# Kernel tuning notes

Measured on AMD Instinct MI355X. Metric: run time of the kernel, lower is better.

Reference implementation:

```python
import jax, jax.numpy as jnp
import numpy as np

B, S, D, H, DH = 2, 2048, 1024, 16, 64
SCALE = float(np.sqrt(DH))
IGNORE = -100000.0


def setup_inputs() -> dict:
    key = jax.random.key(0)
    ks = jax.random.split(key, 9)
    s = 0.02
    return {
        "x": jax.random.normal(ks[0], (B, S, D), dtype=jnp.float32),
        "W_Q": jax.random.normal(ks[1], (H, DH, D), dtype=jnp.float32) * s,
        "W_K": jax.random.normal(ks[2], (H, DH, D), dtype=jnp.float32) * s,
        "W_V": jax.random.normal(ks[3], (H, DH, D), dtype=jnp.float32) * s,
        "W_O": jax.random.normal(ks[4], (H, D, DH), dtype=jnp.float32) * s,
        "b_Q": jax.random.normal(ks[5], (H, DH), dtype=jnp.float32) * s,
        "b_K": jax.random.normal(ks[6], (H, DH), dtype=jnp.float32) * s,
        "b_V": jax.random.normal(ks[7], (H, DH), dtype=jnp.float32) * s,
        "b_O": jax.random.normal(ks[8], (D,), dtype=jnp.float32) * s,
        "mask": jnp.tril(jnp.ones((S, S), dtype=bool)),  # causal, global attn_type
    }


def reference(x, W_Q, W_K, W_V, W_O, b_Q, b_K, b_V, b_O, mask):
    # q,k,v: [batch, pos, head, d_head]
    q = jnp.einsum('ihm,bpm->bpih', W_Q, x) + b_Q
    k = jnp.einsum('ihm,bpm->bpih', W_K, x) + b_K
    v = jnp.einsum('ihm,bpm->bpih', W_V, x) + b_V
    # scores: [batch, head, q_pos, k_pos]
    attn_scores = jnp.einsum('bpih,bqih->bipq', q, k) / SCALE
    attn_scores = jnp.where(mask, attn_scores, IGNORE)
    attn = jax.nn.softmax(attn_scores, axis=-1)
    # z: [batch, q_pos, head, d_head]
    z = jnp.einsum('bpih,biqp->bqih', v, attn)
    out = jnp.einsum('idh,bqih->bqd', W_O, z) + b_O
    return out
```

## Files before the change

kernel.cpp:

```cpp
#include <hip/hip_runtime.h>
#include <stdint.h>

typedef __attribute__((ext_vector_type(8))) short bf16x8;
typedef __attribute__((ext_vector_type(4))) float f32x4;
typedef __attribute__((ext_vector_type(16))) float f32x16;
typedef __attribute__((ext_vector_type(4))) unsigned short us4;

#define LOG2E 1.44269504088896340736f

__device__ __forceinline__ unsigned short f2bf(float f) {
    union { float f; unsigned u; } v; v.f = f;
    unsigned r = v.u + 0x7FFFu + ((v.u >> 16) & 1u);
    return (unsigned short)(r >> 16);
}
__device__ __forceinline__ float bf2f(unsigned short u) {
    return __uint_as_float(((unsigned)u) << 16);
}

__device__ __forceinline__ unsigned cvtpk(float lo, float hi) {
    unsigned r;
    asm("v_cvt_pk_bf16_f32 %0, %1, %2" : "=v"(r) : "v"(lo), "v"(hi));
    return r;
}
__device__ __forceinline__ void plswap(unsigned &a, unsigned &b) {
    asm volatile("v_permlane32_swap_b32 %0, %1" : "+v"(a), "+v"(b));
}

__device__ __forceinline__ void gld16(const void* g, void* l) {
    __builtin_amdgcn_global_load_lds((const __attribute__((address_space(1))) void*)g,
                                     (__attribute__((address_space(3))) void*)l, 16, 0, 0);
}

__global__ void k_cvt(const float* __restrict__ in, unsigned short* __restrict__ out, int n4) {
    int i = blockIdx.x * blockDim.x + threadIdx.x;
    if (i >= n4) return;
    float4 v = ((const float4*)in)[i];
    us4 o; o.x = f2bf(v.x); o.y = f2bf(v.y); o.z = f2bf(v.z); o.w = f2bf(v.w);
    *(us4*)(out + (size_t)i * 4) = o;
}

__global__ void k_cvt_wo(const float* __restrict__ WO, unsigned short* __restrict__ out) {
    int t = blockIdx.x * blockDim.x + threadIdx.x;
    int d = t >> 10, nn = t & 1023, i = nn >> 6, h = nn & 63;
    out[t] = f2bf(WO[(((size_t)i << 10) + d) * 64 + h]);
}

__global__ __launch_bounds__(256) void k_gemm_qkv(
    const unsigned short* __restrict__ Xb,
    const unsigned short* __restrict__ Wq, const unsigned short* __restrict__ Wk,
    const unsigned short* __restrict__ Wv,
    const float* __restrict__ bQ, const float* __restrict__ bK, const float* __restrict__ bV,
    unsigned short* __restrict__ Qb, unsigned short* __restrict__ Kb, unsigned short* __restrict__ VTb)
{
    __shared__ unsigned short As[128][64];
    __shared__ unsigned short Bs[128][64];
    const int which = blockIdx.z;
    const unsigned short* Wp = which == 0 ? Wq : (which == 1 ? Wk : Wv);
    const int bm = blockIdx.x, bn = blockIdx.y;
    const int t = threadIdx.x, lane = t & 63, wave = t >> 6;
    const int wm = wave >> 1, wn = wave & 1;
    const int l15 = lane & 15, l4 = lane >> 4;
    const int rsw = l15 & 7;
    f32x4 acc[4][4] = {};
    for (int k0 = 0; k0 < 1024; k0 += 64) {
        #pragma unroll
        for (int it = 0; it < 4; ++it) {
            int c = it * 256 + wave * 64 + lane;
            int row = c >> 3, sl = (c & 7) ^ (row & 7);
            gld16(Xb + ((bm << 7) + row) * 1024 + k0 + sl * 8, (char*)As + ((it * 256 + wave * 64) << 4));
            gld16(Wp + ((bn << 7) + row) * 1024 + k0 + sl * 8, (char*)Bs + ((it * 256 + wave * 64) << 4));
        }
        __syncthreads();
        const char* Ab = (const char*)As;
        const char* Bb = (const char*)Bs;
        #pragma unroll
        for (int kk = 0; kk < 2; ++kk) {
            bf16x8 af[4], bfg[4];
            #pragma unroll
            for (int m = 0; m < 4; ++m)
                af[m] = *(const bf16x8*)(Ab + (wm * 64 + m * 16 + l15) * 128 + (((kk * 4 + l4) ^ rsw) << 4));
            #pragma unroll
            for (int n = 0; n < 4; ++n)
                bfg[n] = *(const bf16x8*)(Bb + (wn * 64 + n * 16 + l15) * 128 + (((kk * 4 + l4) ^ rsw) << 4));
            #pragma unroll
            for (int m = 0; m < 4; ++m)
                #pragma unroll
                for (int n = 0; n < 4; ++n)
                    acc[m][n] = __builtin_amdgcn_mfma_f32_16x16x32_bf16(af[m], bfg[n], acc[m][n], 0, 0, 0);
        }
        __syncthreads();
    }
    #pragma unroll
    for (int m = 0; m < 4; ++m) {
        #pragma unroll
        for (int n = 0; n < 4; ++n) {
            int col = (bn << 7) + wn * 64 + n * 16 + l15;
            int i = col >> 6, h = col & 63;
            float bias = which == 0 ? bQ[col] : (which == 1 ? bK[col] : bV[col]);
            #pragma unroll
            for (int r = 0; r < 4; ++r) {
                int p = (bm << 7) + wm * 64 + m * 16 + (l4 << 2) + r;
                int b = p >> 11, s = p & 2047;
                float v = acc[m][n][r] + bias;
                if (which == 0)
                    Qb[(((((size_t)b << 4) + i) << 11) + s) * 64 + h] = f2bf(v * (0.125f * LOG2E));
                else if (which == 1)
                    Kb[(((((size_t)b << 4) + i) << 11) + s) * 64 + h] = f2bf(v);
                else
                    VTb[(((((size_t)b << 4) + i) << 6) + h) * 2048 + s] = f2bf(v);
            }
        }
    }
}

__global__ __launch_bounds__(128) void k_attn(
    const unsigned short* __restrict__ Qb, const unsigned short* __restrict__ Kb,
    const unsigned short* __restrict__ VTb,
    unsigned short* __restrict__ Zp, float* __restrict__ Lse)
{
    __shared__ __align__(16) char Lbuf[16384];
    const int id = (int)blockIdx.x;
    const int bi = id & 31;
    const int r = id >> 5;
    const int c = 31 - (r >> 1);
    const int part = r & 1;
    const int n = c + 1, n0 = (n + 1) >> 1;
    const int t0 = part ? n0 : 0, t1 = part ? n : n0;
    const int lane = threadIdx.x & 63, w = threadIdx.x >> 6;
    const int l31 = lane & 31, hi = lane >> 5;
    const unsigned short* Qh = Qb + (size_t)bi * 2048 * 64;
    const char* Khb = (const char*)(Kb + (size_t)bi * 2048 * 64);
    const char* Vhb = (const char*)(VTb + (size_t)bi * 64 * 2048);
    const int q0 = c * 64 + w * 32;
    const int q = q0 + l31;

    bf16x8 qf[4];
    #pragma unroll
    for (int kk = 0; kk < 4; ++kk)
        qf[kk] = *(const bf16x8*)&Qh[(size_t)q * 64 + kk * 16 + hi * 8];

    const int r8 = lane >> 3;
    const int swz = ((lane & 7) * 16) ^ (r8 << 4);
    const int koff = r8 * 128 + swz;
    const int voff = r8 * 4096 + swz;

    const int rsw = (l31 & 7) << 4;
    int kaddr[8];
    #pragma unroll
    for (int i = 0; i < 8; ++i)
        kaddr[i] = (l31 + 32 * (i >> 2)) * 128 + ((32 * (i & 3) + 16 * hi) ^ rsw);
    int vcol[4];
    #pragma unroll
    for (int f = 0; f < 4; ++f)
        vcol[f] = ((f * 32 + 16 * hi) ^ rsw);

    f32x16 za0 = {}, za1 = {};
    float m_run = -1e30f, l_run = 0.f;

    if (t0 < t1) {
        if (w == 0) {
            const char* src = Khb + (size_t)t0 * 8192 + koff;
            #pragma unroll
            for (int it = 0; it < 8; ++it) gld16(src + it * 1024, &Lbuf[0] + it * 1024);
        } else {
            const char* src = Vhb + (size_t)t0 * 128 + voff;
            #pragma unroll
            for (int it = 0; it < 8; ++it) gld16(src + it * 32768, &Lbuf[8192] + it * 1024);
        }
    }

    for (int t = t0; t < t1; ++t) {
        __syncthreads();
        const char* KL = &Lbuf[0];
        const char* VL = &Lbuf[8192];
        bf16x8 ka[8];
        #pragma unroll
        for (int i = 0; i < 8; ++i) ka[i] = *(const bf16x8*)(KL + kaddr[i]);
        bf16x8 vf0[4], vf1[4];
        #pragma unroll
        for (int f = 0; f < 4; ++f) {
            vf0[f] = *(const bf16x8*)(VL + l31 * 128 + vcol[f]);
            vf1[f] = *(const bf16x8*)(VL + (l31 + 32) * 128 + vcol[f]);
        }
        __syncthreads();
        if (t + 1 < t1) {
            if (w == 0) {
                const char* src = Khb + (size_t)(t + 1) * 8192 + koff;
                #pragma unroll
                for (int it = 0; it < 8; ++it) gld16(src + it * 1024, &Lbuf[0] + it * 1024);
            } else {
                const char* src = Vhb + (size_t)(t + 1) * 128 + voff;
                #pragma unroll
                for (int it = 0; it < 8; ++it) gld16(src + it * 32768, &Lbuf[8192] + it * 1024);
            }
        }

        const bool full = !(t == c && w == 0);
        f32x16 s0 = {}, s1;
        __builtin_amdgcn_s_setprio(1);
        #pragma unroll
        for (int kk = 0; kk < 4; ++kk)
            s0 = __builtin_amdgcn_mfma_f32_32x32x16_bf16(ka[kk], qf[kk], s0, 0, 0, 0);
        if (full) {
            f32x16 z = {};
            #pragma unroll
            for (int kk = 0; kk < 4; ++kk)
                z = __builtin_amdgcn_mfma_f32_32x32x16_bf16(ka[4 + kk], qf[kk], z, 0, 0, 0);
            s1 = z;
        }
        __builtin_amdgcn_s_setprio(0);

        if (!full) {
            #pragma unroll
            for (int j = 0; j < 16; ++j) s1[j] = -100000.0f;
        }
        if (t == c) {
            #pragma unroll
            for (int j = 0; j < 16; ++j) {
                int kv0 = (j & 3) + 8 * (j >> 2) + 4 * hi;
                if (c * 64 + kv0 > q) s0[j] = -100000.0f;
                if (c * 64 + kv0 + 32 > q) s1[j] = -100000.0f;
            }
        }
        float tmax = -1e30f;
        #pragma unroll
        for (int j = 0; j < 16; ++j) tmax = fmaxf(tmax, fmaxf(s0[j], s1[j]));
        tmax = fmaxf(tmax, __shfl_xor(tmax, 32, 64));
        if (!__all(tmax <= m_run + 8.0f)) {
            float newm = fmaxf(m_run, tmax);
            float alpha = exp2f(m_run - newm);
            m_run = newm;
            l_run *= alpha;
            za0 *= alpha; za1 *= alpha;
        }
        float rsum = 0.f;
        #pragma unroll
        for (int j = 0; j < 16; ++j) { s0[j] = exp2f(s0[j] - m_run); rsum += s0[j]; }
        if (full) {
            #pragma unroll
            for (int j = 0; j < 16; ++j) { s1[j] = exp2f(s1[j] - m_run); rsum += s1[j]; }
        }
        rsum += __shfl_xor(rsum, 32, 64);
        l_run += rsum;

        union { unsigned u[4]; bf16x8 v; } pk0, pk1, pk2, pk3;
        {
            unsigned a0 = cvtpk(s0[0], s0[1]),  a1 = cvtpk(s0[2], s0[3]);
            unsigned a2 = cvtpk(s0[4], s0[5]),  a3 = cvtpk(s0[6], s0[7]);
            plswap(a0, a2); plswap(a1, a3);
            pk0.u[0] = a0; pk0.u[1] = a1; pk0.u[2] = a2; pk0.u[3] = a3;
            unsigned b0 = cvtpk(s0[8], s0[9]),  b1 = cvtpk(s0[10], s0[11]);
            unsigned b2 = cvtpk(s0[12], s0[13]), b3 = cvtpk(s0[14], s0[15]);
            plswap(b0, b2); plswap(b1, b3);
            pk1.u[0] = b0; pk1.u[1] = b1; pk1.u[2] = b2; pk1.u[3] = b3;
        }
        if (full) {
            unsigned a0 = cvtpk(s1[0], s1[1]),  a1 = cvtpk(s1[2], s1[3]);
            unsigned a2 = cvtpk(s1[4], s1[5]),  a3 = cvtpk(s1[6], s1[7]);
            plswap(a0, a2); plswap(a1, a3);
            pk2.u[0] = a0; pk2.u[1] = a1; pk2.u[2] = a2; pk2.u[3] = a3;
            unsigned b0 = cvtpk(s1[8], s1[9]),  b1 = cvtpk(s1[10], s1[11]);
            unsigned b2 = cvtpk(s1[12], s1[13]), b3 = cvtpk(s1[14], s1[15]);
            plswap(b0, b2); plswap(b1, b3);
            pk3.u[0] = b0; pk3.u[1] = b1; pk3.u[2] = b2; pk3.u[3] = b3;
        }
        __builtin_amdgcn_s_setprio(1);
        za0 = __builtin_amdgcn_mfma_f32_32x32x16_bf16(vf0[0], pk0.v, za0, 0, 0, 0);
        za1 = __builtin_amdgcn_mfma_f32_32x32x16_bf16(vf1[0], pk0.v, za1, 0, 0, 0);
        za0 = __builtin_amdgcn_mfma_f32_32x32x16_bf16(vf0[1], pk1.v, za0, 0, 0, 0);
        za1 = __builtin_amdgcn_mfma_f32_32x32x16_bf16(vf1[1], pk1.v, za1, 0, 0, 0);
        if (full) {
            za0 = __builtin_amdgcn_mfma_f32_32x32x16_bf16(vf0[2], pk2.v, za0, 0, 0, 0);
            za1 = __builtin_amdgcn_mfma_f32_32x32x16_bf16(vf1[2], pk2.v, za1, 0, 0, 0);
            za0 = __builtin_amdgcn_mfma_f32_32x32x16_bf16(vf0[3], pk3.v, za0, 0, 0, 0);
            za1 = __builtin_amdgcn_mfma_f32_32x32x16_bf16(vf1[3], pk3.v, za1, 0, 0, 0);
        }
        __builtin_amdgcn_s_setprio(0);
    }

    const float rl = (l_run > 0.f) ? 1.0f / l_run : 0.f;
    const float lse = (l_run > 0.f) ? m_run + log2f(l_run) : -1e30f;
    const int pb = (part << 5) + bi;
    unsigned short* zp = Zp + ((size_t)pb * 2048 + q) * 64;
    #pragma unroll
    for (int nn = 0; nn < 2; ++nn) {
        #pragma unroll
        for (int gg = 0; gg < 4; ++gg) {
            int dh0 = nn * 32 + 8 * gg + 4 * hi;
            us4 o;
            float v0 = (nn ? za1[4 * gg + 0] : za0[4 * gg + 0]) * rl;
            float v1 = (nn ? za1[4 * gg + 1] : za0[4 * gg + 1]) * rl;
            float v2 = (nn ? za1[4 * gg + 2] : za0[4 * gg + 2]) * rl;
            float v3 = (nn ? za1[4 * gg + 3] : za0[4 * gg + 3]) * rl;
            o.x = f2bf(v0); o.y = f2bf(v1); o.z = f2bf(v2); o.w = f2bf(v3);
            *(us4*)(zp + dh0) = o;
        }
    }
    if (hi == 0) Lse[(size_t)pb * 2048 + q] = lse;
}

__global__ __launch_bounds__(256) void k_combine(
    const unsigned short* __restrict__ Zp, const float* __restrict__ Lse,
    unsigned short* __restrict__ Zb)
{
    const int tid = blockIdx.x * 256 + threadIdx.x;
    const int dc = tid & 7, q = (tid >> 3) & 2047, bi = tid >> 14;
    const float l0 = Lse[(size_t)bi * 2048 + q];
    const float l1 = Lse[(size_t)(32 + bi) * 2048 + q];
    const float M = fmaxf(l0, l1);
    float e0 = exp2f(l0 - M), e1 = exp2f(l1 - M);
    const float rs = 1.0f / (e0 + e1);
    e0 *= rs; e1 *= rs;
    const size_t base = ((size_t)bi * 2048 + q) * 64 + dc * 8;
    bf16x8 z0 = *(const bf16x8*)(Zp + base);
    bf16x8 z1 = *(const bf16x8*)(Zp + (size_t)32 * 2048 * 64 + base);
    const int b = bi >> 4, ih = bi & 15;
    unsigned short* op = Zb + (((size_t)b * 2048 + q) << 10) + ih * 64 + dc * 8;
    bf16x8 o;
    #pragma unroll
    for (int j = 0; j < 8; ++j) {
        float v = e0 * bf2f((unsigned short)z0[j]) + e1 * bf2f((unsigned short)z1[j]);
        o[j] = (short)f2bf(v);
    }
    *(bf16x8*)op = o;
}

__global__ __launch_bounds__(256) void k_gemm_out(
    const unsigned short* __restrict__ Zb, const unsigned short* __restrict__ Wo,
    const float* __restrict__ bO, float* __restrict__ out)
{
    __shared__ unsigned short As[128][64];
    __shared__ unsigned short Bs[128][64];
    const int bm = blockIdx.x, bn = blockIdx.y;
    const int t = threadIdx.x, lane = t & 63, wave = t >> 6;
    const int wm = wave >> 1, wn = wave & 1;
    const int l15 = lane & 15, l4 = lane >> 4;
    const int rsw = l15 & 7;
    f32x4 acc[4][4] = {};
    for (int k0 = 0; k0 < 1024; k0 += 64) {
        #pragma unroll
        for (int it = 0; it < 4; ++it) {
            int c = it * 256 + wave * 64 + lane;
            int row = c >> 3, sl = (c & 7) ^ (row & 7);
            gld16(Zb + ((bm << 7) + row) * 1024 + k0 + sl * 8, (char*)As + ((it * 256 + wave * 64) << 4));
            gld16(Wo + ((bn << 7) + row) * 1024 + k0 + sl * 8, (char*)Bs + ((it * 256 + wave * 64) << 4));
        }
        __syncthreads();
        const char* Ab = (const char*)As;
        const char* Bb = (const char*)Bs;
        #pragma unroll
        for (int kk = 0; kk < 2; ++kk) {
            bf16x8 af[4], bfg[4];
            #pragma unroll
            for (int m = 0; m < 4; ++m)
                af[m] = *(const bf16x8*)(Ab + (wm * 64 + m * 16 + l15) * 128 + (((kk * 4 + l4) ^ rsw) << 4));
            #pragma unroll
            for (int n = 0; n < 4; ++n)
                bfg[n] = *(const bf16x8*)(Bb + (wn * 64 + n * 16 + l15) * 128 + (((kk * 4 + l4) ^ rsw) << 4));
            #pragma unroll
            for (int m = 0; m < 4; ++m)
                #pragma unroll
                for (int n = 0; n < 4; ++n)
                    acc[m][n] = __builtin_amdgcn_mfma_f32_16x16x32_bf16(af[m], bfg[n], acc[m][n], 0, 0, 0);
        }
        __syncthreads();
    }
    #pragma unroll
    for (int m = 0; m < 4; ++m) {
        #pragma unroll
        for (int n = 0; n < 4; ++n) {
            int col = (bn << 7) + wn * 64 + n * 16 + l15;
            float bias = bO[col];
            #pragma unroll
            for (int r = 0; r < 4; ++r) {
                int p = (bm << 7) + wm * 64 + m * 16 + (l4 << 2) + r;
                out[(size_t)p * 1024 + col] = acc[m][n][r] + bias;
            }
        }
    }
}

extern "C" void kernel_launch(void* const* d_in, const int* in_sizes, int n_in,
                              void* d_out, int out_size, void* d_ws, size_t ws_size,
                              hipStream_t stream)
{
    const float* x  = (const float*)d_in[0];
    const float* WQ = (const float*)d_in[1];
    const float* WK = (const float*)d_in[2];
    const float* WV = (const float*)d_in[3];
    const float* WO = (const float*)d_in[4];
    const float* bQ = (const float*)d_in[5];
    const float* bK = (const float*)d_in[6];
    const float* bV = (const float*)d_in[7];
    const float* bO = (const float*)d_in[8];
    float* out = (float*)d_out;

    char* w = (char*)d_ws;
    unsigned short* xb  = (unsigned short*)w; w += (size_t)4096 * 1024 * 2;
    unsigned short* wqb = (unsigned short*)w; w += (size_t)1024 * 1024 * 2;
    unsigned short* wkb = (unsigned short*)w; w += (size_t)1024 * 1024 * 2;
    unsigned short* wvb = (unsigned short*)w; w += (size_t)1024 * 1024 * 2;
    unsigned short* wob = (unsigned short*)w; w += (size_t)1024 * 1024 * 2;
    unsigned short* Qb  = (unsigned short*)w; w += (size_t)4096 * 1024 * 2;
    unsigned short* Kb  = (unsigned short*)w; w += (size_t)4096 * 1024 * 2;
    unsigned short* VTb = (unsigned short*)w; w += (size_t)4096 * 1024 * 2;
    unsigned short* Zb  = (unsigned short*)w; w += (size_t)4096 * 1024 * 2;
    unsigned short* Zp  = (unsigned short*)w; w += (size_t)2 * 32 * 2048 * 64 * 2;
    float*          Lse = (float*)w;          w += (size_t)2 * 32 * 2048 * 4;

    k_cvt<<<4096, 256, 0, stream>>>(x, xb, 1048576);
    k_cvt<<<1024, 256, 0, stream>>>(WQ, wqb, 262144);
    k_cvt<<<1024, 256, 0, stream>>>(WK, wkb, 262144);
    k_cvt<<<1024, 256, 0, stream>>>(WV, wvb, 262144);
    k_cvt_wo<<<4096, 256, 0, stream>>>(WO, wob);

    k_gemm_qkv<<<dim3(32, 8, 3), 256, 0, stream>>>(xb, wqb, wkb, wvb, bQ, bK, bV, Qb, Kb, VTb);
    k_attn<<<2048, 128, 0, stream>>>(Qb, Kb, VTb, Zp, Lse);
    k_combine<<<2048, 256, 0, stream>>>(Zp, Lse, Zb);
    k_gemm_out<<<dim3(32, 8), 256, 0, stream>>>(Zb, wob, bO, out);
}
```

Measured before the change: 141.1 us.

## Double-buffer LDS tiles in QKV and output GEMMs, merge weight conversions

Both projection GEMMs now use two LDS buffers, so the global-to-LDS loads for the next K-slice are issued before the MFMA work on the current slice, overlapping memory latency with compute. One barrier per iteration is dropped. The three Q/K/V weight conversion launches are merged into a single 2D-grid launch to cut launch overhead. LDS use per block doubles to 64KB, which may reduce the number of blocks resident per CU.

```diff
diff --git a/kernel.cpp b/kernel.cpp
--- a/kernel.cpp
+++ b/kernel.cpp
@@ -34,6 +34,18 @@
 __global__ void k_cvt(const float* __restrict__ in, unsigned short* __restrict__ out, int n4) {
     int i = blockIdx.x * blockDim.x + threadIdx.x;
     if (i >= n4) return;
+    float4 v = ((const float4*)in)[i];
+    us4 o; o.x = f2bf(v.x); o.y = f2bf(v.y); o.z = f2bf(v.z); o.w = f2bf(v.w);
+    *(us4*)(out + (size_t)i * 4) = o;
+}
+
+__global__ void k_cvt3(const float* __restrict__ a, const float* __restrict__ b,
+                       const float* __restrict__ cc,
+                       unsigned short* __restrict__ oa, unsigned short* __restrict__ ob,
+                       unsigned short* __restrict__ oc) {
+    const float* in = blockIdx.y == 0 ? a : (blockIdx.y == 1 ? b : cc);
+    unsigned short* out = blockIdx.y == 0 ? oa : (blockIdx.y == 1 ? ob : oc);
+    int i = blockIdx.x * blockDim.x + threadIdx.x;
     float4 v = ((const float4*)in)[i];
     us4 o; o.x = f2bf(v.x); o.y = f2bf(v.y); o.z = f2bf(v.z); o.w = f2bf(v.w);
     *(us4*)(out + (size_t)i * 4) = o;
@@ -52,8 +64,8 @@
     const float* __restrict__ bQ, const float* __restrict__ bK, const float* __restrict__ bV,
     unsigned short* __restrict__ Qb, unsigned short* __restrict__ Kb, unsigned short* __restrict__ VTb)
 {
-    __shared__ unsigned short As[128][64];
-    __shared__ unsigned short Bs[128][64];
+    __shared__ unsigned short As[2][128][64];
+    __shared__ unsigned short Bs[2][128][64];
     const int which = blockIdx.z;
     const unsigned short* Wp = which == 0 ? Wq : (which == 1 ? Wk : Wv);
     const int bm = blockIdx.x, bn = blockIdx.y;
@@ -61,18 +73,33 @@
     const int wm = wave >> 1, wn = wave & 1;
     const int l15 = lane & 15, l4 = lane >> 4;
     const int rsw = l15 & 7;
+
+    const int c0 = wave * 64 + lane;
     f32x4 acc[4][4] = {};
-    for (int k0 = 0; k0 < 1024; k0 += 64) {
-        #pragma unroll
-        for (int it = 0; it < 4; ++it) {
-            int c = it * 256 + wave * 64 + lane;
-            int row = c >> 3, sl = (c & 7) ^ (row & 7);
-            gld16(Xb + ((bm << 7) + row) * 1024 + k0 + sl * 8, (char*)As + ((it * 256 + wave * 64) << 4));
-            gld16(Wp + ((bn << 7) + row) * 1024 + k0 + sl * 8, (char*)Bs + ((it * 256 + wave * 64) << 4));
-        }
-        __syncthreads();
-        const char* Ab = (const char*)As;
-        const char* Bb = (const char*)Bs;
+
+    #pragma unroll
+    for (int it = 0; it < 4; ++it) {
+        int c = it * 256 + c0;
+        int row = c >> 3, sl = (c & 7) ^ (row & 7);
+        gld16(Xb + ((bm << 7) + row) * 1024 + 0 + sl * 8, (char*)&As[0][0][0] + ((it * 256 + c0) << 4));
+        gld16(Wp + ((bn << 7) + row) * 1024 + 0 + sl * 8, (char*)&Bs[0][0][0] + ((it * 256 + c0) << 4));
+    }
+    __syncthreads();
+
+    int cur = 0;
+    for (int ks = 0; ks < 16; ++ks) {
+        if (ks < 15) {
+            const int k0 = (ks + 1) << 6;
+            #pragma unroll
+            for (int it = 0; it < 4; ++it) {
+                int c = it * 256 + c0;
+                int row = c >> 3, sl = (c & 7) ^ (row & 7);
+                gld16(Xb + ((bm << 7) + row) * 1024 + k0 + sl * 8, (char*)&As[cur ^ 1][0][0] + ((it * 256 + c0) << 4));
+                gld16(Wp + ((bn << 7) + row) * 1024 + k0 + sl * 8, (char*)&Bs[cur ^ 1][0][0] + ((it * 256 + c0) << 4));
+            }
+        }
+        const char* Ab = (const char*)&As[cur][0][0];
+        const char* Bb = (const char*)&Bs[cur][0][0];
         #pragma unroll
         for (int kk = 0; kk < 2; ++kk) {
             bf16x8 af[4], bfg[4];
@@ -89,6 +116,7 @@
                     acc[m][n] = __builtin_amdgcn_mfma_f32_16x16x32_bf16(af[m], bfg[n], acc[m][n], 0, 0, 0);
         }
         __syncthreads();
+        cur ^= 1;
     }
     #pragma unroll
     for (int m = 0; m < 4; ++m) {
@@ -329,25 +357,39 @@
     const unsigned short* __restrict__ Zb, const unsigned short* __restrict__ Wo,
     const float* __restrict__ bO, float* __restrict__ out)
 {
-    __shared__ unsigned short As[128][64];
-    __shared__ unsigned short Bs[128][64];
+    __shared__ unsigned short As[2][128][64];
+    __shared__ unsigned short Bs[2][128][64];
     const int bm = blockIdx.x, bn = blockIdx.y;
     const int t = threadIdx.x, lane = t & 63, wave = t >> 6;
     const int wm = wave >> 1, wn = wave & 1;
     const int l15 = lane & 15, l4 = lane >> 4;
     const int rsw = l15 & 7;
+    const int c0 = wave * 64 + lane;
     f32x4 acc[4][4] = {};
-    for (int k0 = 0; k0 < 1024; k0 += 64) {
-        #pragma unroll
-        for (int it = 0; it < 4; ++it) {
-            int c = it * 256 + wave * 64 + lane;
-            int row = c >> 3, sl = (c & 7) ^ (row & 7);
-            gld16(Zb + ((bm << 7) + row) * 1024 + k0 + sl * 8, (char*)As + ((it * 256 + wave * 64) << 4));
-            gld16(Wo + ((bn << 7) + row) * 1024 + k0 + sl * 8, (char*)Bs + ((it * 256 + wave * 64) << 4));
-        }
-        __syncthreads();
-        const char* Ab = (const char*)As;
-        const char* Bb = (const char*)Bs;
+
+    #pragma unroll
+    for (int it = 0; it < 4; ++it) {
+        int c = it * 256 + c0;
+        int row = c >> 3, sl = (c & 7) ^ (row & 7);
+        gld16(Zb + ((bm << 7) + row) * 1024 + 0 + sl * 8, (char*)&As[0][0][0] + ((it * 256 + c0) << 4));
+        gld16(Wo + ((bn << 7) + row) * 1024 + 0 + sl * 8, (char*)&Bs[0][0][0] + ((it * 256 + c0) << 4));
+    }
+    __syncthreads();
+
+    int cur = 0;
+    for (int ks = 0; ks < 16; ++ks) {
+        if (ks < 15) {
+            const int k0 = (ks + 1) << 6;
+            #pragma unroll
+            for (int it = 0; it < 4; ++it) {
+                int c = it * 256 + c0;
+                int row = c >> 3, sl = (c & 7) ^ (row & 7);
+                gld16(Zb + ((bm << 7) + row) * 1024 + k0 + sl * 8, (char*)&As[cur ^ 1][0][0] + ((it * 256 + c0) << 4));
+                gld16(Wo + ((bn << 7) + row) * 1024 + k0 + sl * 8, (char*)&Bs[cur ^ 1][0][0] + ((it * 256 + c0) << 4));
+            }
+        }
+        const char* Ab = (const char*)&As[cur][0][0];
+        const char* Bb = (const char*)&Bs[cur][0][0];
         #pragma unroll
         for (int kk = 0; kk < 2; ++kk) {
             bf16x8 af[4], bfg[4];
@@ -364,6 +406,7 @@
                     acc[m][n] = __builtin_amdgcn_mfma_f32_16x16x32_bf16(af[m], bfg[n], acc[m][n], 0, 0, 0);
         }
         __syncthreads();
+        cur ^= 1;
     }
     #pragma unroll
     for (int m = 0; m < 4; ++m) {
@@ -409,9 +452,7 @@
     float*          Lse = (float*)w;          w += (size_t)2 * 32 * 2048 * 4;
 
     k_cvt<<<4096, 256, 0, stream>>>(x, xb, 1048576);
-    k_cvt<<<1024, 256, 0, stream>>>(WQ, wqb, 262144);
-    k_cvt<<<1024, 256, 0, stream>>>(WK, wkb, 262144);
-    k_cvt<<<1024, 256, 0, stream>>>(WV, wvb, 262144);
+    k_cvt3<<<dim3(1024, 3), 256, 0, stream>>>(WQ, WK, WV, wqb, wkb, wvb);
     k_cvt_wo<<<4096, 256, 0, stream>>>(WO, wob);
 
     k_gemm_qkv<<<dim3(32, 8, 3), 256, 0, stream>>>(xb, wqb, wkb, wvb, bQ, bK, bV, Qb, Kb, VTb);
```

New measurement: 138.5 us. About the same (-1.9%).
